# Kernel optimization log

Measured on AMD Instinct MI355X. Metric: run time of the kernel, lower is better.

## Reference

```python
import jax, jax.numpy as jnp
import numpy as np

N_NODES = 50000
N_EDGES = 800000
IN_FEATS = 64
HIDDEN = 64
NUM_CLASSES = 32


def _graph_conv(x, src, dst, W, b, n_nodes):
    # DGL GraphConv, norm='both', allow_zero_in_degree=True:
    # out = D_in^{-1/2} * (A^T @ (D_out^{-1/2} * x)) @ W + b, degrees clamped to >=1
    e = src.shape[0]
    ones = jnp.ones((e,), dtype=x.dtype)
    out_deg = jax.ops.segment_sum(ones, src, num_segments=n_nodes)
    in_deg = jax.ops.segment_sum(ones, dst, num_segments=n_nodes)
    norm_src = jax.lax.rsqrt(jnp.maximum(out_deg, 1.0))[:, None]
    norm_dst = jax.lax.rsqrt(jnp.maximum(in_deg, 1.0))[:, None]
    h = x * norm_src                                   # [N, d]
    agg = jax.ops.segment_sum(h[src], dst, num_segments=n_nodes)  # gather+scatter over edges
    return (agg * norm_dst) @ W + b


def setup_inputs() -> dict:
    key = jax.random.key(0)
    k1, k2, k3, k4, k5 = jax.random.split(key, 5)
    features = jax.random.normal(k1, (N_NODES, IN_FEATS), dtype=jnp.float32)
    src = jax.random.randint(k2, (N_EDGES,), 0, N_NODES, dtype=jnp.int32)
    dst = jax.random.randint(k3, (N_EDGES,), 0, N_NODES, dtype=jnp.int32)
    W1 = jax.random.normal(k4, (IN_FEATS, HIDDEN), dtype=jnp.float32) * (1.0 / np.sqrt(IN_FEATS))
    b1 = jnp.zeros((HIDDEN,), dtype=jnp.float32)
    W2 = jax.random.normal(k5, (HIDDEN, NUM_CLASSES), dtype=jnp.float32) * (1.0 / np.sqrt(HIDDEN))
    b2 = jnp.zeros((NUM_CLASSES,), dtype=jnp.float32)
    return {"features": features, "src": src, "dst": dst,
            "W1": W1, "b1": b1, "W2": W2, "b2": b2}


def reference(features, src, dst, W1, b1, W2, b2) -> jnp.ndarray:
    n = features.shape[0]
    h = jax.nn.relu(_graph_conv(features, src, dst, W1, b1, n))
    out = _graph_conv(h, src, dst, W2, b2, n)
    # single canonical etype -> mean over one-element stack is identity
    return out
```

## Files before the change

kernel.cpp:

```cpp
#include <hip/hip_runtime.h>
#include <hip/hip_bf16.h>

#define N_NODES 50000
#define N_EDGES 800000
#define F 64
#define C 32
#define CAP 48

#define NPB   200
#define EPB   4000
#define NBUCK 196

static __device__ __forceinline__ float bf2f(unsigned short u) {
    return __uint_as_float(((unsigned)u) << 16);
}
static __device__ __forceinline__ unsigned short f2bf(float f) {
    __hip_bfloat16 h = __float2bfloat16(f);
    return *reinterpret_cast<unsigned short*>(&h);
}

__global__ void part_count_kernel(const int* __restrict__ src, const int* __restrict__ dst,
                                  int* __restrict__ bcnt_d, int* __restrict__ bcnt_s) {
    __shared__ int hd[NBUCK], hs[NBUCK];
    int t = threadIdx.x;
    for (int i = t; i < NBUCK; i += 256) { hd[i] = 0; hs[i] = 0; }
    __syncthreads();
    int b0 = blockIdx.x * EPB;
    for (int i = b0 + t; i < b0 + EPB; i += 256) {
        atomicAdd(&hd[dst[i] >> 8], 1);
        atomicAdd(&hs[src[i] >> 8], 1);
    }
    __syncthreads();
    for (int i = t; i < NBUCK; i += 256) {
        bcnt_d[blockIdx.x * NBUCK + i] = hd[i];
        bcnt_s[blockIdx.x * NBUCK + i] = hs[i];
    }
}

__global__ void part_scan_kernel(const int* __restrict__ bcnt_d, const int* __restrict__ bcnt_s,
                                 int* __restrict__ eoff_d, int* __restrict__ eoff_s,
                                 int* __restrict__ base_d, int* __restrict__ base_s) {
    __shared__ int tot_d[NBUCK], tot_s[NBUCK], bd[NBUCK + 1], bs[NBUCK + 1];
    int t = threadIdx.x;
    if (t < NBUCK) {
        int run = 0;
        for (int blk = 0; blk < NPB; blk++) {
            eoff_d[blk * NBUCK + t] = run;
            run += bcnt_d[blk * NBUCK + t];
        }
        tot_d[t] = run;
        run = 0;
        for (int blk = 0; blk < NPB; blk++) {
            eoff_s[blk * NBUCK + t] = run;
            run += bcnt_s[blk * NBUCK + t];
        }
        tot_s[t] = run;
    }
    __syncthreads();
    if (t == 0) {
        int r = 0;
        for (int b = 0; b < NBUCK; b++) { bd[b] = r; r += tot_d[b]; }
        bd[NBUCK] = r;
        r = 0;
        for (int b = 0; b < NBUCK; b++) { bs[b] = r; r += tot_s[b]; }
        bs[NBUCK] = r;
    }
    __syncthreads();
    if (t < NBUCK + 1) { base_d[t] = bd[t]; base_s[t] = bs[t]; }
}

__global__ void part_scatter_kernel(const int* __restrict__ src, const int* __restrict__ dst,
                                    const int* __restrict__ eoff_d, const int* __restrict__ eoff_s,
                                    const int* __restrict__ base_d, const int* __restrict__ base_s,
                                    int* __restrict__ edge_d, int* __restrict__ edge_s) {
    __shared__ int cd[NBUCK], cs[NBUCK];
    int t = threadIdx.x;
    for (int i = t; i < NBUCK; i += 256) {
        cd[i] = base_d[i] + eoff_d[blockIdx.x * NBUCK + i];
        cs[i] = base_s[i] + eoff_s[blockIdx.x * NBUCK + i];
    }
    __syncthreads();
    int b0 = blockIdx.x * EPB;
    for (int i = b0 + t; i < b0 + EPB; i += 256) {
        int d = dst[i], s = src[i];
        int p = atomicAdd(&cd[d >> 8], 1);
        edge_d[p] = ((d & 255) << 16) | s;
        int q = atomicAdd(&cs[s >> 8], 1);
        edge_s[q] = s & 255;
    }
}

__global__ void bucket_build_kernel(const int* __restrict__ edge_d, const int* __restrict__ edge_s,
                                    const int* __restrict__ base_d, const int* __restrict__ base_s,
                                    int* __restrict__ csr, int* __restrict__ cnt,
                                    float* __restrict__ norm_dst, float* __restrict__ norm_src) {
    __shared__ int cur[256];
    __shared__ int hs[256];
    int t = threadIdx.x;
    int bucket = blockIdx.x;
    cur[t] = 0;
    hs[t] = 0;
    __syncthreads();
    int lo = base_d[bucket], hi = base_d[bucket + 1];
    for (int i = lo + t; i < hi; i += 256) {
        int pd = edge_d[i];
        int dlow = pd >> 16;
        int s = pd & 0xFFFF;
        int pos = atomicAdd(&cur[dlow], 1);
        if (pos < CAP) csr[(size_t)(bucket * 256 + dlow) * CAP + pos] = s;
    }
    int slo = base_s[bucket], shi = base_s[bucket + 1];
    for (int i = slo + t; i < shi; i += 256) {
        atomicAdd(&hs[edge_s[i]], 1);
    }
    __syncthreads();
    int node = bucket * 256 + t;
    if (node < N_NODES) {
        int c = cur[t] < CAP ? cur[t] : CAP;
        cnt[node] = c;
        norm_dst[node] = rsqrtf(fmaxf((float)c, 1.0f));
        norm_src[node] = rsqrtf(fmaxf((float)hs[t], 1.0f));
    }
}

__global__ void gemm_y_kernel(const float* __restrict__ x,
                              const float* __restrict__ ns,
                              const float* __restrict__ W,
                              __hip_bfloat16* __restrict__ y) {
    __shared__ float sW[F * F];
    __shared__ float srow[16][F];
    int t = threadIdx.x;
    for (int i = t; i < F * F; i += 256) sW[i] = W[i];
    int j = t & 63;
    int w = t >> 6;
    int base = blockIdx.x * 16;
    for (int r = w; r < 16; r += 4) srow[r][j] = x[(size_t)(base + r) * F + j];
    __syncthreads();
    float a0 = 0, a1 = 0, a2 = 0, a3 = 0;
#pragma unroll
    for (int k = 0; k < F; k++) {
        float wv = sW[k * F + j];
        a0 += srow[w * 4 + 0][k] * wv;
        a1 += srow[w * 4 + 1][k] * wv;
        a2 += srow[w * 4 + 2][k] * wv;
        a3 += srow[w * 4 + 3][k] * wv;
    }
    int n0 = base + w * 4;
    y[(size_t)(n0 + 0) * F + j] = __float2bfloat16(a0 * ns[n0 + 0]);
    y[(size_t)(n0 + 1) * F + j] = __float2bfloat16(a1 * ns[n0 + 1]);
    y[(size_t)(n0 + 2) * F + j] = __float2bfloat16(a2 * ns[n0 + 2]);
    y[(size_t)(n0 + 3) * F + j] = __float2bfloat16(a3 * ns[n0 + 3]);
}

struct f4 { float x, y, z, w; };

static __device__ __forceinline__ void gacc(const __hip_bfloat16* __restrict__ tab,
                                            int s, int fo, f4& a) {
    const ushort4 v = *reinterpret_cast<const ushort4*>(
        reinterpret_cast<const unsigned short*>(tab) + (size_t)s * F + fo);
    a.x += bf2f(v.x); a.y += bf2f(v.y); a.z += bf2f(v.z); a.w += bf2f(v.w);
}

__global__ void gather64_kernel(const __hip_bfloat16* __restrict__ y,
                                const int* __restrict__ csr,
                                const int* __restrict__ cnt,
                                const float* __restrict__ norm_dst,
                                const float* __restrict__ norm_src,
                                const float* __restrict__ b1,
                                __hip_bfloat16* __restrict__ h2) {
    int gid  = blockIdx.x * blockDim.x + threadIdx.x;
    int node = gid >> 6;
    int lane = threadIdx.x & 63;
    if (node >= N_NODES) return;
    int g  = lane >> 4;
    int fo = (lane & 15) * 4;
    int n = cnt[node];
    const int* row = csr + (size_t)node * CAP;
    f4 a = {0.f, 0.f, 0.f, 0.f};
    int e = 0;
    if (e + 15 < n) {
        int4 idx = *reinterpret_cast<const int4*>(row + e + 4 * g);
        for (; e + 31 < n; e += 16) {
            int4 nxt = *reinterpret_cast<const int4*>(row + e + 16 + 4 * g);
            gacc(y, idx.x, fo, a);
            gacc(y, idx.y, fo, a);
            gacc(y, idx.z, fo, a);
            gacc(y, idx.w, fo, a);
            idx = nxt;
        }
        gacc(y, idx.x, fo, a);
        gacc(y, idx.y, fo, a);
        gacc(y, idx.z, fo, a);
        gacc(y, idx.w, fo, a);
        e += 16;
    }
    for (; e < n; e += 4) {
        int ee = e + g;
        if (ee < n) gacc(y, row[ee], fo, a);
    }
    a.x += __shfl_down(a.x, 16); a.y += __shfl_down(a.y, 16);
    a.z += __shfl_down(a.z, 16); a.w += __shfl_down(a.w, 16);
    a.x += __shfl_down(a.x, 32); a.y += __shfl_down(a.y, 32);
    a.z += __shfl_down(a.z, 32); a.w += __shfl_down(a.w, 32);
    if (lane < 16) {
        float nd = norm_dst[node], ns = norm_src[node];
        unsigned long long pk =
            ((unsigned long long)f2bf(fmaxf(a.x * nd + b1[fo + 0], 0.0f) * ns)) |
            ((unsigned long long)f2bf(fmaxf(a.y * nd + b1[fo + 1], 0.0f) * ns) << 16) |
            ((unsigned long long)f2bf(fmaxf(a.z * nd + b1[fo + 2], 0.0f) * ns) << 32) |
            ((unsigned long long)f2bf(fmaxf(a.w * nd + b1[fo + 3], 0.0f) * ns) << 48);
        __builtin_nontemporal_store(pk, reinterpret_cast<unsigned long long*>(
            reinterpret_cast<unsigned short*>(h2) + (size_t)node * F + fo));
    }
}

__global__ void gather_gemm2_kernel(const __hip_bfloat16* __restrict__ h2,
                                    const int* __restrict__ csr,
                                    const int* __restrict__ cnt,
                                    const float* __restrict__ norm_dst,
                                    const float* __restrict__ W2,
                                    const float* __restrict__ b2,
                                    float* __restrict__ out) {
    __shared__ float sW[F * C];
    __shared__ float sagg[4][F];
    int t = threadIdx.x;
    for (int i = t; i < F * C; i += 256) sW[i] = W2[i];
    int w    = t >> 6;
    int lane = t & 63;
    int node = blockIdx.x * 4 + w;
    int g  = lane >> 4;
    int fo = (lane & 15) * 4;
    f4 a = {0.f, 0.f, 0.f, 0.f};
    if (node < N_NODES) {
        int n = cnt[node];
        const int* row = csr + (size_t)node * CAP;
        int e = 0;
        if (e + 15 < n) {
            int4 idx = *reinterpret_cast<const int4*>(row + e + 4 * g);
            for (; e + 31 < n; e += 16) {
                int4 nxt = *reinterpret_cast<const int4*>(row + e + 16 + 4 * g);
                gacc(h2, idx.x, fo, a);
                gacc(h2, idx.y, fo, a);
                gacc(h2, idx.z, fo, a);
                gacc(h2, idx.w, fo, a);
                idx = nxt;
            }
            gacc(h2, idx.x, fo, a);
            gacc(h2, idx.y, fo, a);
            gacc(h2, idx.z, fo, a);
            gacc(h2, idx.w, fo, a);
            e += 16;
        }
        for (; e < n; e += 4) {
            int ee = e + g;
            if (ee < n) gacc(h2, row[ee], fo, a);
        }
    }
    a.x += __shfl_down(a.x, 16); a.y += __shfl_down(a.y, 16);
    a.z += __shfl_down(a.z, 16); a.w += __shfl_down(a.w, 16);
    a.x += __shfl_down(a.x, 32); a.y += __shfl_down(a.y, 32);
    a.z += __shfl_down(a.z, 32); a.w += __shfl_down(a.w, 32);
    if (lane < 16) {
        sagg[w][fo + 0] = a.x;
        sagg[w][fo + 1] = a.y;
        sagg[w][fo + 2] = a.z;
        sagg[w][fo + 3] = a.w;
    }
    __syncthreads();
    int j    = lane & 31;
    int half = lane >> 5;
    float o = 0.0f;
    if (node < N_NODES) {
#pragma unroll
        for (int k = 0; k < 32; k++) {
            int kk = half * 32 + k;
            o += sagg[w][kk] * sW[kk * C + j];
        }
    }
    o += __shfl_down(o, 32);
    if (node < N_NODES && half == 0)
        __builtin_nontemporal_store(o * norm_dst[node] + b2[j],
                                    &out[(size_t)node * C + j]);
}

extern "C" void kernel_launch(void* const* d_in, const int* in_sizes, int n_in,
                              void* d_out, int out_size, void* d_ws, size_t ws_size,
                              hipStream_t stream) {
    const float* features = (const float*)d_in[0];
    const int*   src      = (const int*)d_in[1];
    const int*   dst      = (const int*)d_in[2];
    const float* W1       = (const float*)d_in[3];
    const float* b1       = (const float*)d_in[4];
    const float* W2       = (const float*)d_in[5];
    const float* b2       = (const float*)d_in[6];
    float* out = (float*)d_out;

    char* p = (char*)d_ws;
    float* norm_src = (float*)p;  p += (size_t)N_NODES * 4;
    float* norm_dst = (float*)p;  p += (size_t)N_NODES * 4;
    int*   cnt      = (int*)p;    p += (size_t)N_NODES * 4;
    int*   csr      = (int*)p;    p += (size_t)N_NODES * CAP * 4;
    __hip_bfloat16* y  = (__hip_bfloat16*)p;  p += (size_t)N_NODES * F * 2;
    __hip_bfloat16* h2 = (__hip_bfloat16*)p;

    int* edge_d = (int*)y;
    int* edge_s = edge_d + N_EDGES;
    int* q = (int*)h2;
    int* bcnt_d = q;                 q += NPB * NBUCK;
    int* bcnt_s = q;                 q += NPB * NBUCK;
    int* eoff_d = q;                 q += NPB * NBUCK;
    int* eoff_s = q;                 q += NPB * NBUCK;
    int* base_d = q;                 q += NBUCK + 1;
    int* base_s = q;

    part_count_kernel<<<NPB, 256, 0, stream>>>(src, dst, bcnt_d, bcnt_s);
    part_scan_kernel<<<1, 256, 0, stream>>>(bcnt_d, bcnt_s, eoff_d, eoff_s, base_d, base_s);
    part_scatter_kernel<<<NPB, 256, 0, stream>>>(src, dst, eoff_d, eoff_s, base_d, base_s,
                                                 edge_d, edge_s);
    bucket_build_kernel<<<NBUCK, 256, 0, stream>>>(edge_d, edge_s, base_d, base_s,
                                                   csr, cnt, norm_dst, norm_src);

    gemm_y_kernel<<<N_NODES / 16, 256, 0, stream>>>(features, norm_src, W1, y);
    gather64_kernel<<<(N_NODES * 64) / 256, 256, 0, stream>>>(y, csr, cnt, norm_dst,
                                                              norm_src, b1, h2);

    gather_gemm2_kernel<<<(N_NODES + 3) / 4, 256, 0, stream>>>(h2, csr, cnt, norm_dst,
                                                               W2, b2, out);
}
```

Baseline: 213.6 us.

## Apply second-layer weight before aggregation to gather 32-wide rows instead of 64

The second GraphConv now multiplies by W2 before aggregating, using linearity. The first gather kernel applies ReLU and norm_src and then the 64x32 GEMV per node, storing a 32-wide bf16 table. The final gather then reads half as many bytes per edge. The cost is an extra bf16 rounding after the GEMV and moving the W2 shared-memory load and block sync into the first gather kernel.

```diff
diff --git a/kernel.cpp b/kernel.cpp
--- a/kernel.cpp
+++ b/kernel.cpp
@@ -153,6 +153,7 @@
 }
 
 struct f4 { float x, y, z, w; };
+struct f2 { float x, y; };
 
 static __device__ __forceinline__ void gacc(const __hip_bfloat16* __restrict__ tab,
                                             int s, int fo, f4& a) {
@@ -160,18 +161,27 @@
         reinterpret_cast<const unsigned short*>(tab) + (size_t)s * F + fo);
     a.x += bf2f(v.x); a.y += bf2f(v.y); a.z += bf2f(v.z); a.w += bf2f(v.w);
 }
-
-__global__ void gather64_kernel(const __hip_bfloat16* __restrict__ y,
-                                const int* __restrict__ csr,
-                                const int* __restrict__ cnt,
-                                const float* __restrict__ norm_dst,
-                                const float* __restrict__ norm_src,
-                                const float* __restrict__ b1,
-                                __hip_bfloat16* __restrict__ h2) {
-    int gid  = blockIdx.x * blockDim.x + threadIdx.x;
-    int node = gid >> 6;
-    int lane = threadIdx.x & 63;
-    if (node >= N_NODES) return;
+static __device__ __forceinline__ void gacc2(const unsigned short* __restrict__ tab,
+                                             int s, int fo, f2& a) {
+    const ushort2 v = *reinterpret_cast<const ushort2*>(tab + (size_t)s * C + fo);
+    a.x += bf2f(v.x); a.y += bf2f(v.y);
+}
+
+__global__ void gather64_gemv_kernel(const __hip_bfloat16* __restrict__ y,
+                                     const int* __restrict__ csr,
+                                     const int* __restrict__ cnt,
+                                     const float* __restrict__ norm_dst,
+                                     const float* __restrict__ norm_src,
+                                     const float* __restrict__ b1,
+                                     const float* __restrict__ W2,
+                                     __hip_bfloat16* __restrict__ gt) {
+    __shared__ float sW[F * C];
+    __shared__ float sagg[4][F];
+    int t = threadIdx.x;
+    for (int i = t; i < F * C; i += 256) sW[i] = W2[i];
+    int w    = t >> 6;
+    int lane = t & 63;
+    int node = blockIdx.x * 4 + w;
     int g  = lane >> 4;
     int fo = (lane & 15) * 4;
     int n = cnt[node];
@@ -204,83 +214,74 @@
     a.z += __shfl_down(a.z, 32); a.w += __shfl_down(a.w, 32);
     if (lane < 16) {
         float nd = norm_dst[node], ns = norm_src[node];
-        unsigned long long pk =
-            ((unsigned long long)f2bf(fmaxf(a.x * nd + b1[fo + 0], 0.0f) * ns)) |
-            ((unsigned long long)f2bf(fmaxf(a.y * nd + b1[fo + 1], 0.0f) * ns) << 16) |
-            ((unsigned long long)f2bf(fmaxf(a.z * nd + b1[fo + 2], 0.0f) * ns) << 32) |
-            ((unsigned long long)f2bf(fmaxf(a.w * nd + b1[fo + 3], 0.0f) * ns) << 48);
-        __builtin_nontemporal_store(pk, reinterpret_cast<unsigned long long*>(
-            reinterpret_cast<unsigned short*>(h2) + (size_t)node * F + fo));
-    }
-}
-
-__global__ void gather_gemm2_kernel(const __hip_bfloat16* __restrict__ h2,
-                                    const int* __restrict__ csr,
-                                    const int* __restrict__ cnt,
-                                    const float* __restrict__ norm_dst,
-                                    const float* __restrict__ W2,
-                                    const float* __restrict__ b2,
-                                    float* __restrict__ out) {
-    __shared__ float sW[F * C];
-    __shared__ float sagg[4][F];
-    int t = threadIdx.x;
-    for (int i = t; i < F * C; i += 256) sW[i] = W2[i];
-    int w    = t >> 6;
-    int lane = t & 63;
-    int node = blockIdx.x * 4 + w;
-    int g  = lane >> 4;
-    int fo = (lane & 15) * 4;
-    f4 a = {0.f, 0.f, 0.f, 0.f};
-    if (node < N_NODES) {
-        int n = cnt[node];
-        const int* row = csr + (size_t)node * CAP;
-        int e = 0;
-        if (e + 15 < n) {
-            int4 idx = *reinterpret_cast<const int4*>(row + e + 4 * g);
-            for (; e + 31 < n; e += 16) {
-                int4 nxt = *reinterpret_cast<const int4*>(row + e + 16 + 4 * g);
-                gacc(h2, idx.x, fo, a);
-                gacc(h2, idx.y, fo, a);
-                gacc(h2, idx.z, fo, a);
-                gacc(h2, idx.w, fo, a);
-                idx = nxt;
-            }
-            gacc(h2, idx.x, fo, a);
-            gacc(h2, idx.y, fo, a);
-            gacc(h2, idx.z, fo, a);
-            gacc(h2, idx.w, fo, a);
-            e += 16;
-        }
-        for (; e < n; e += 4) {
-            int ee = e + g;
-            if (ee < n) gacc(h2, row[ee], fo, a);
-        }
-    }
-    a.x += __shfl_down(a.x, 16); a.y += __shfl_down(a.y, 16);
-    a.z += __shfl_down(a.z, 16); a.w += __shfl_down(a.w, 16);
-    a.x += __shfl_down(a.x, 32); a.y += __shfl_down(a.y, 32);
-    a.z += __shfl_down(a.z, 32); a.w += __shfl_down(a.w, 32);
-    if (lane < 16) {
-        sagg[w][fo + 0] = a.x;
-        sagg[w][fo + 1] = a.y;
-        sagg[w][fo + 2] = a.z;
-        sagg[w][fo + 3] = a.w;
+        sagg[w][fo + 0] = fmaxf(a.x * nd + b1[fo + 0], 0.0f) * ns;
+        sagg[w][fo + 1] = fmaxf(a.y * nd + b1[fo + 1], 0.0f) * ns;
+        sagg[w][fo + 2] = fmaxf(a.z * nd + b1[fo + 2], 0.0f) * ns;
+        sagg[w][fo + 3] = fmaxf(a.w * nd + b1[fo + 3], 0.0f) * ns;
     }
     __syncthreads();
     int j    = lane & 31;
     int half = lane >> 5;
     float o = 0.0f;
-    if (node < N_NODES) {
 #pragma unroll
-        for (int k = 0; k < 32; k++) {
-            int kk = half * 32 + k;
-            o += sagg[w][kk] * sW[kk * C + j];
+    for (int k = 0; k < 32; k++) {
+        int kk = half * 32 + k;
+        o += sagg[w][kk] * sW[kk * C + j];
+    }
+    o += __shfl_down(o, 32);
+    if (half == 0)
+        __builtin_nontemporal_store(f2bf(o),
+            reinterpret_cast<unsigned short*>(gt) + (size_t)node * C + j);
+}
+
+__global__ void gather_out_kernel(const __hip_bfloat16* __restrict__ gt,
+                                  const int* __restrict__ csr,
+                                  const int* __restrict__ cnt,
+                                  const float* __restrict__ norm_dst,
+                                  const float* __restrict__ b2,
+                                  float* __restrict__ out) {
+    int gid  = blockIdx.x * blockDim.x + threadIdx.x;
+    int node = gid >> 6;
+    if (node >= N_NODES) return;
+    int lane = threadIdx.x & 63;
+    int g  = lane >> 4;
+    int fo = (lane & 15) * 2;
+    const unsigned short* tab = reinterpret_cast<const unsigned short*>(gt);
+    int n = cnt[node];
+    const int* row = csr + (size_t)node * CAP;
+    f2 a = {0.f, 0.f};
+    int e = 0;
+    if (e + 15 < n) {
+        int4 idx = *reinterpret_cast<const int4*>(row + e + 4 * g);
+        for (; e + 31 < n; e += 16) {
+            int4 nxt = *reinterpret_cast<const int4*>(row + e + 16 + 4 * g);
+            gacc2(tab, idx.x, fo, a);
+            gacc2(tab, idx.y, fo, a);
+            gacc2(tab, idx.z, fo, a);
+            gacc2(tab, idx.w, fo, a);
+            idx = nxt;
         }
-    }
-    o += __shfl_down(o, 32);
-    if (node < N_NODES && half == 0)
-        __builtin_nontemporal_store(o * norm_dst[node] + b2[j],
-                                    &out[(size_t)node * C + j]);
+        gacc2(tab, idx.x, fo, a);
+        gacc2(tab, idx.y, fo, a);
+        gacc2(tab, idx.z, fo, a);
+        gacc2(tab, idx.w, fo, a);
+        e += 16;
+    }
+    for (; e < n; e += 4) {
+        int ee = e + g;
+        if (ee < n) gacc2(tab, row[ee], fo, a);
+    }
+    a.x += __shfl_down(a.x, 16); a.y += __shfl_down(a.y, 16);
+    a.x += __shfl_down(a.x, 32); a.y += __shfl_down(a.y, 32);
+    if (lane < 16) {
+        float nd = norm_dst[node];
+        float ox = a.x * nd + b2[fo + 0];
+        float oy = a.y * nd + b2[fo + 1];
+        unsigned long long pk = ((unsigned long long)__float_as_uint(ox)) |
+                                ((unsigned long long)__float_as_uint(oy) << 32);
+        __builtin_nontemporal_store(pk, reinterpret_cast<unsigned long long*>(
+            out + (size_t)node * C + fo));
+    }
 }
 
 extern "C" void kernel_launch(void* const* d_in, const int* in_sizes, int n_in,
@@ -301,11 +302,11 @@
     int*   cnt      = (int*)p;    p += (size_t)N_NODES * 4;
     int*   csr      = (int*)p;    p += (size_t)N_NODES * CAP * 4;
     __hip_bfloat16* y  = (__hip_bfloat16*)p;  p += (size_t)N_NODES * F * 2;
-    __hip_bfloat16* h2 = (__hip_bfloat16*)p;
+    __hip_bfloat16* gt = (__hip_bfloat16*)p;
 
     int* edge_d = (int*)y;
     int* edge_s = edge_d + N_EDGES;
-    int* q = (int*)h2;
+    int* q = (int*)gt;
     int* bcnt_d = q;                 q += NPB * NBUCK;
     int* bcnt_s = q;                 q += NPB * NBUCK;
     int* eoff_d = q;                 q += NPB * NBUCK;
@@ -321,9 +322,9 @@
                                                    csr, cnt, norm_dst, norm_src);
 
     gemm_y_kernel<<<N_NODES / 16, 256, 0, stream>>>(features, norm_src, W1, y);
-    gather64_kernel<<<(N_NODES * 64) / 256, 256, 0, stream>>>(y, csr, cnt, norm_dst,
-                                                              norm_src, b1, h2);
-
-    gather_gemm2_kernel<<<(N_NODES + 3) / 4, 256, 0, stream>>>(h2, csr, cnt, norm_dst,
-                                                               W2, b2, out);
-}
+    gather64_gemv_kernel<<<N_NODES / 4, 256, 0, stream>>>(y, csr, cnt, norm_dst,
+                                                          norm_src, b1, W2, gt);
+
+    gather_out_kernel<<<(N_NODES * 64) / 256, 256, 0, stream>>>(gt, csr, cnt, norm_dst,
+                                                                b2, out);
+}
```

After: 206.2 us. 1.04x faster.
